# Kernel tuning notes

Measured on AMD Instinct MI355X. Metric: run time of the kernel, lower is better.

Reference implementation:

```python
import jax, jax.numpy as jnp
import numpy as np

MAX_PERIOD = 10000.0


def _rope(x, ts):
    # x: [B,H,T,D], ts: [B,T] integer positions (per-batch offset + arange(T))
    B, H, T, D = x.shape
    half = D // 2
    freqs = jnp.exp(jnp.arange(half, dtype=jnp.float32) * (-np.log(MAX_PERIOD) * 2.0 / D))
    ang = ts.astype(jnp.float32)[:, None, :, None] * freqs  # [B,1,T,half]
    cos, sin = jnp.cos(ang), jnp.sin(ang)
    xr = x.reshape(B, H, T, half, 2)  # interleaved (real, imag) pairs
    r, i = xr[..., 0], xr[..., 1]
    out = jnp.stack([r * cos - i * sin, r * sin + i * cos], axis=-1)
    return out.reshape(B, H, T, D)


def setup_inputs() -> dict:
    key = jax.random.key(0)
    ks = jax.random.split(key, 7)
    B, T, C = 8, 128, 1024
    H, D, CAP = 16, 64, 2048
    return {
        'x': jax.random.normal(ks[0], (B, T, C), dtype=jnp.float32),
        'w_in': jax.random.normal(ks[1], (3 * C, C), dtype=jnp.float32) * 0.02,
        'w_out': jax.random.normal(ks[2], (C, C), dtype=jnp.float32) * 0.02,
        'cache_k': jax.random.normal(ks[3], (B, H, CAP, D), dtype=jnp.float32),
        'cache_v': jax.random.normal(ks[4], (B, H, CAP, D), dtype=jnp.float32),
        'end_offset': jax.random.randint(ks[5], (B,), 0, CAP).astype(jnp.int64) if jax.config.jax_enable_x64 else jax.random.randint(ks[5], (B,), 0, CAP),
        'exec_mask': jnp.ones((B,), dtype=bool),
    }


def reference(x, w_in, w_out, cache_k, cache_v, end_offset, exec_mask):
    B, T, C = x.shape
    H, CAP = cache_k.shape[1], cache_k.shape[2]
    D = C // H
    context = CAP  # capacity == self.context

    # fused in-projection, split per rearrange 'b t (p h d) -> p b h t d', p=3
    qkv = (x @ w_in.T).reshape(B, T, 3, H, D).transpose(2, 0, 3, 1, 4)
    q, k, v = qkv[0], qkv[1], qkv[2]  # each [B,H,T,D]

    ts = end_offset[:, None] + jnp.arange(T)  # [B,T] absolute positions of new tokens
    q = _rope(q, ts)
    k = _rope(k, ts)

    # ring-buffer scatter (RingKVCache.complete)
    idx = ts % CAP  # [B,T]
    bI = jnp.arange(B)[:, None, None]
    hI = jnp.arange(H)[None, :, None]
    cache_k = cache_k.at[bI, hI, idx[:, None, :]].set(k)
    cache_v = cache_v.at[bI, hI, idx[:, None, :]].set(v)

    # absolute position of every cache slot, -1 for invalid slots
    cap_idx = jnp.arange(CAP)
    last = end_offset + T - 1  # [B]
    end_index = last % CAP
    delta = cap_idx[None, :] - end_index[:, None]  # [B,CAP]
    positions = jnp.where(delta <= 0, last[:, None] + delta, last[:, None] + delta - CAP)
    new_end = jnp.where(exec_mask, end_offset + T, end_offset)
    positions = jnp.where(cap_idx[None, :] >= new_end[:, None], -1, positions)

    # causal + context mask derived from positions
    d = ts[:, :, None] - positions[:, None, :]  # [B,T,CAP]
    mask = (positions[:, None, :] >= 0) & (d >= 0) & (d < context)

    scale = 1.0 / np.sqrt(D)
    scores = jnp.einsum('bhtd,bhsd->bhts', q, cache_k) * scale  # [B,H,T,CAP]
    scores = jnp.where(mask[:, None], scores, jnp.asarray(-1e9, scores.dtype))
    attn = jax.nn.softmax(scores, axis=-1)
    out = jnp.einsum('bhts,bhsd->bhtd', attn, cache_v)
    out = out.transpose(0, 2, 1, 3).reshape(B, T, C)  # 'b h t d -> b t (h d)'
    return out @ w_out.T
```

## Files before the change

kernel.cpp:

```cpp
#include <hip/hip_runtime.h>
#include <math.h>

#define BB 8
#define TT 128
#define CC 1024
#define HH 16
#define DD 64
#define CAP 2048
#define NSPLIT 4

typedef __attribute__((ext_vector_type(8))) short short8;
typedef __attribute__((ext_vector_type(4))) short short4v;
typedef __attribute__((ext_vector_type(4))) float float4v;
typedef _Float16 half8 __attribute__((ext_vector_type(8)));
typedef _Float16 half4v __attribute__((ext_vector_type(4)));

__device__ __forceinline__ short f2bf(float x) {
    union { float f; unsigned u; } un; un.f = x;
    unsigned r = (un.u + 0x7FFF + ((un.u >> 16) & 1)) >> 16;
    return (short)r;
}
__device__ __forceinline__ unsigned cvt_pk_bf16(float a, float b) {
    unsigned r;
    asm("v_cvt_pk_bf16_f32 %0, %1, %2" : "=v"(r) : "v"(a), "v"(b));
    return r;
}

__global__ __launch_bounds__(256) void split_all(const float* __restrict__ x,
                                                 const float* __restrict__ w_in,
                                                 const float* __restrict__ w_out,
                                                 _Float16* __restrict__ xhi,
                                                 _Float16* __restrict__ xlo,
                                                 _Float16* __restrict__ wh,
                                                 _Float16* __restrict__ woh) {
    size_t i = ((size_t)blockIdx.x * 256 + threadIdx.x) * 4;
    if (i < (size_t)1048576) {
        float4 f = *(const float4*)(x + i);
        half4v h, l;
        h.x = (_Float16)f.x; l.x = (_Float16)(f.x - (float)h.x);
        h.y = (_Float16)f.y; l.y = (_Float16)(f.y - (float)h.y);
        h.z = (_Float16)f.z; l.z = (_Float16)(f.z - (float)h.z);
        h.w = (_Float16)f.w; l.w = (_Float16)(f.w - (float)h.w);
        *(half4v*)(xhi + i) = h;
        *(half4v*)(xlo + i) = l;
    } else if (i < (size_t)4194304) {
        size_t off = i - 1048576;
        float4 f = *(const float4*)(w_in + off);
        half4v h;
        h.x = (_Float16)f.x; h.y = (_Float16)f.y; h.z = (_Float16)f.z; h.w = (_Float16)f.w;
        *(half4v*)(wh + off) = h;
    } else {
        size_t off = i - 4194304;
        float4 f = *(const float4*)(w_out + off);
        half4v h;
        h.x = (_Float16)f.x; h.y = (_Float16)f.y; h.z = (_Float16)f.z; h.w = (_Float16)f.w;
        *(half4v*)(woh + off) = h;
    }
}

template <int ROWS>
__device__ __forceinline__ void stage_glds(const unsigned short* __restrict__ src,
                                           unsigned short* lds, int K, int wv, int lane) {
#pragma unroll
    for (int c = wv; c < ROWS / 16; c += 4) {
        int row = c * 16 + (lane >> 2);
        int g = lane & 3;
        const unsigned short* ga = src + (size_t)row * K + g * 8;
        unsigned short* la = lds + c * 512 + lane * 8;
        __builtin_amdgcn_global_load_lds((__attribute__((address_space(1))) const unsigned short*)ga,
                                         (__attribute__((address_space(3))) unsigned short*)la,
                                         16, 0, 0);
    }
}

template <int MT, int NT>
__global__ __launch_bounds__(256) void gemm_f16x2(const _Float16* __restrict__ Ahi,
                                                  const _Float16* __restrict__ Alo,
                                                  const _Float16* __restrict__ Bh,
                                                  float* __restrict__ C, int M, int N, int K) {
    constexpr int BM = 2 * MT * 16, BN = 2 * NT * 16;
    __shared__ __align__(16) _Float16 As_h[BM * 32];
    __shared__ __align__(16) _Float16 As_l[BM * 32];
    __shared__ __align__(16) _Float16 Bs[BN * 32];

    int tid = threadIdx.x;
    int lane = tid & 63, wv = tid >> 6;
    int wr = wv >> 1, wc = wv & 1;
    int quad = lane >> 4, lq = lane & 15;
    int m0 = blockIdx.y * BM, n0 = blockIdx.x * BN;

    float4v acc[MT][NT];
#pragma unroll
    for (int mt = 0; mt < MT; ++mt)
#pragma unroll
        for (int nt = 0; nt < NT; ++nt) acc[mt][nt] = (float4v){0.f, 0.f, 0.f, 0.f};

    const unsigned short* a_h = (const unsigned short*)(Ahi + (size_t)m0 * K);
    const unsigned short* a_l = (const unsigned short*)(Alo + (size_t)m0 * K);
    const unsigned short* b_h = (const unsigned short*)(Bh + (size_t)n0 * K);

    for (int k0 = 0; k0 < K; k0 += 32) {
        __syncthreads();
        stage_glds<BM>(a_h + k0, (unsigned short*)As_h, K, wv, lane);
        stage_glds<BM>(a_l + k0, (unsigned short*)As_l, K, wv, lane);
        stage_glds<BN>(b_h + k0, (unsigned short*)Bs, K, wv, lane);
        __syncthreads();

        half8 ah[MT], al[MT];
#pragma unroll
        for (int mt = 0; mt < MT; ++mt) {
            int row = wr * MT * 16 + mt * 16 + lq;
            ah[mt] = *(const half8*)&As_h[row * 32 + quad * 8];
            al[mt] = *(const half8*)&As_l[row * 32 + quad * 8];
        }
#pragma unroll
        for (int nt = 0; nt < NT; ++nt) {
            int row = wc * NT * 16 + nt * 16 + lq;
            half8 bh = *(const half8*)&Bs[row * 32 + quad * 8];
#pragma unroll
            for (int mt = 0; mt < MT; ++mt) {
                float4v c = acc[mt][nt];
                c = __builtin_amdgcn_mfma_f32_16x16x32_f16(ah[mt], bh, c, 0, 0, 0);
                c = __builtin_amdgcn_mfma_f32_16x16x32_f16(al[mt], bh, c, 0, 0, 0);
                acc[mt][nt] = c;
            }
        }
    }

#pragma unroll
    for (int mt = 0; mt < MT; ++mt)
#pragma unroll
        for (int nt = 0; nt < NT; ++nt) {
            int n = n0 + wc * NT * 16 + nt * 16 + lq;
#pragma unroll
            for (int r = 0; r < 4; ++r) {
                int m = m0 + wr * MT * 16 + mt * 16 + quad * 4 + r;
                C[(size_t)m * N + n] = acc[mt][nt][r];
            }
        }
}

__global__ __launch_bounds__(256) void rope_scatter(const float* __restrict__ qkv,
                                                    unsigned short* __restrict__ q_bf,
                                                    float* __restrict__ cache_k,
                                                    float* __restrict__ cache_v,
                                                    const int* __restrict__ end_offset) {
    int gid = blockIdx.x * 256 + threadIdx.x;
    int j = gid & 31;
    int h = (gid >> 5) & 15;
    int t = (gid >> 9) & 127;
    int b = gid >> 16;

    int ts = end_offset[b] + t;
    int slot = ts & (CAP - 1);

    float freq = expf(-0.28782313662425574f * (float)j);
    float ang = (float)ts * freq;
    float s, c;
    sincosf(ang, &s, &c);

    const float* base = qkv + (size_t)(b * TT + t) * (3 * CC);
    int col = h * DD + 2 * j;
    float2 qv = *(const float2*)&base[col];
    float2 kv = *(const float2*)&base[CC + col];
    float2 vv = *(const float2*)&base[2 * CC + col];

    float qr = qv.x * c - qv.y * s;
    float qi = qv.x * s + qv.y * c;
    float kr = kv.x * c - kv.y * s;
    float ki = kv.x * s + kv.y * c;

    size_t qo = ((size_t)(b * HH + h) * TT + t) * DD + 2 * j;
    ushort2 qp;
    qp.x = (unsigned short)f2bf(qr * 0.125f);
    qp.y = (unsigned short)f2bf(qi * 0.125f);
    *(ushort2*)&q_bf[qo] = qp;
    size_t ko = ((size_t)(b * HH + h) * CAP + slot) * DD + 2 * j;
    *(float2*)&cache_k[ko] = make_float2(kr, ki);
    *(float2*)&cache_v[ko] = vv;
}

__global__ __launch_bounds__(256) void attn_mfma(const unsigned short* __restrict__ qb,
                                                 const float* __restrict__ ck,
                                                 const float* __restrict__ cv,
                                                 const int* __restrict__ endo,
                                                 const unsigned char* __restrict__ emb,
                                                 const int* __restrict__ emi,
                                                 float* __restrict__ pacc012,
                                                 float* __restrict__ pacc3,
                                                 float* __restrict__ pml) {
    __shared__ __align__(16) short k_s[64 * 72];
    __shared__ __align__(16) short v_t[64 * 64];
    __shared__ __align__(16) short p_s[4][16 * 72];

    int tid = threadIdx.x;
    int lane = tid & 63, wv = tid >> 6;
    int quad = lane >> 4, lq = lane & 15;
    int f = blockIdx.x + 128 * (blockIdx.y + 2 * blockIdx.z);
    int sid = f & 3;
    int qc2 = (f >> 2) & 1;
    int hb = f >> 3;
    int h = hb & 15, b = hb >> 4;
    int qrow = qc2 * 64 + wv * 16 + lq;

    int end0 = endo[b];
    int em = (emb[b] != 0) || (emi[b] != 0);
    int last = end0 + TT - 1;
    int end_index = last & (CAP - 1);
    int new_end = em ? (end0 + TT) : end0;
    int se = new_end < CAP ? new_end : CAP;
    int ntiles = (se + 63) >> 6;

    int tq = end0 + qrow;
    int tq0 = end0 + qc2 * 64 + wv * 16;
    int len_bad = last - tq0;
    int a_bad = (tq0 + 1) & (CAP - 1);

    const unsigned short* qrp = qb + ((size_t)(b * HH + h) * TT + qrow) * DD;
    short8 aq0 = *(const short8*)(qrp + quad * 8);
    short8 aq1 = *(const short8*)(qrp + 32 + quad * 8);

    const float* kg = ck + (size_t)(b * HH + h) * CAP * DD;
    const float* vg = cv + (size_t)(b * HH + h) * CAP * DD;

    int k_row = tid >> 4, k_f4 = tid & 15;
    float4 kreg[4];
    float vreg[2][8];

    float m = 0.f, l = 0.f;
    float4v acc[4];
#pragma unroll
    for (int mt = 0; mt < 4; ++mt) acc[mt] = (float4v){0.f, 0.f, 0.f, 0.f};

    if (sid < ntiles) {
        int sb = sid * 64;
#pragma unroll
        for (int i = 0; i < 4; ++i)
            kreg[i] = *(const float4*)&kg[(size_t)(sb + k_row + 16 * i) * DD + k_f4 * 4];
#pragma unroll
        for (int gi = 0; gi < 2; ++gi) {
            int g = wv + gi * 4;
#pragma unroll
            for (int i = 0; i < 8; ++i)
                vreg[gi][i] = vg[(size_t)(sb + g * 8 + i) * DD + lane];
        }
    }

    for (int t = sid; t < ntiles; t += NSPLIT) {
        int s0 = t * 64;
        __syncthreads();
#pragma unroll
        for (int i = 0; i < 4; ++i) {
            float4 fv = kreg[i];
            uint2 u;
            u.x = cvt_pk_bf16(fv.x, fv.y);
            u.y = cvt_pk_bf16(fv.z, fv.w);
            *(uint2*)&k_s[(k_row + 16 * i) * 72 + k_f4 * 4] = u;
        }
#pragma unroll
        for (int gi = 0; gi < 2; ++gi) {
            int g = wv + gi * 4;
            uint4 u;
            u.x = cvt_pk_bf16(vreg[gi][0], vreg[gi][1]);
            u.y = cvt_pk_bf16(vreg[gi][2], vreg[gi][3]);
            u.z = cvt_pk_bf16(vreg[gi][4], vreg[gi][5]);
            u.w = cvt_pk_bf16(vreg[gi][6], vreg[gi][7]);
            *(uint4*)&v_t[lane * 64 + (g ^ (lane & 7)) * 8] = u;
        }
        __syncthreads();
        int tn = t + NSPLIT;
        if (tn < ntiles) {
            int sn = tn * 64;
#pragma unroll
            for (int i = 0; i < 4; ++i)
                kreg[i] = *(const float4*)&kg[(size_t)(sn + k_row + 16 * i) * DD + k_f4 * 4];
#pragma unroll
            for (int gi = 0; gi < 2; ++gi) {
                int g = wv + gi * 4;
#pragma unroll
                for (int i = 0; i < 8; ++i)
                    vreg[gi][i] = vg[(size_t)(sn + g * 8 + i) * DD + lane];
            }
        }

        float4v sc[4];
#pragma unroll
        for (int nt = 0; nt < 4; ++nt) {
            const short* kr = &k_s[(nt * 16 + lq) * 72 + quad * 8];
            short8 bk0 = *(const short8*)kr;
            short8 bk1 = *(const short8*)(kr + 32);
            float4v c = (float4v){0.f, 0.f, 0.f, 0.f};
            c = __builtin_amdgcn_mfma_f32_16x16x32_bf16(bk0, aq0, c, 0, 0, 0);
            c = __builtin_amdgcn_mfma_f32_16x16x32_bf16(bk1, aq1, c, 0, 0, 0);
            sc[nt] = c;
        }

        int off = (s0 - a_bad) & (CAP - 1);
        bool fast = (off >= len_bad) && (off <= CAP - 64) && (s0 + 63 < se);
        float x[4][4];
        if (fast) {
#pragma unroll
            for (int nt = 0; nt < 4; ++nt)
#pragma unroll
                for (int r = 0; r < 4; ++r) x[nt][r] = sc[nt][r];
        } else {
#pragma unroll
            for (int nt = 0; nt < 4; ++nt)
#pragma unroll
                for (int r = 0; r < 4; ++r) {
                    int s = s0 + nt * 16 + quad * 4 + r;
                    int delta = s - end_index;
                    int pos = (delta <= 0) ? (last + delta) : (last + delta - CAP);
                    bool valid = (s < se) && (pos <= tq);
                    x[nt][r] = valid ? sc[nt][r] : -1.0e30f;
                }
        }

        float v01 = fmaxf(fmaxf(x[0][0], x[0][1]), fmaxf(x[0][2], x[0][3]));
        float v23 = fmaxf(fmaxf(x[1][0], x[1][1]), fmaxf(x[1][2], x[1][3]));
        float v45 = fmaxf(fmaxf(x[2][0], x[2][1]), fmaxf(x[2][2], x[2][3]));
        float v67 = fmaxf(fmaxf(x[3][0], x[3][1]), fmaxf(x[3][2], x[3][3]));
        float vm = fmaxf(fmaxf(v01, v23), fmaxf(v45, v67));
        vm = fmaxf(vm, __shfl_xor(vm, 16, 64));
        vm = fmaxf(vm, __shfl_xor(vm, 32, 64));
        float mn = fmaxf(m, vm);
        float al = __expf(m - mn);
        float ps = 0.f;
#pragma unroll
        for (int nt = 0; nt < 4; ++nt)
#pragma unroll
            for (int r = 0; r < 4; ++r) {
                float p = __expf(x[nt][r] - mn);
                x[nt][r] = p;
                ps += p;
            }
        ps += __shfl_xor(ps, 16, 64);
        ps += __shfl_xor(ps, 32, 64);
        l = l * al + ps;
        m = mn;

#pragma unroll
        for (int nt = 0; nt < 4; ++nt) {
            uint2 u;
            u.x = cvt_pk_bf16(x[nt][0], x[nt][1]);
            u.y = cvt_pk_bf16(x[nt][2], x[nt][3]);
            *(uint2*)&p_s[wv][lq * 72 + nt * 16 + quad * 4] = u;
        }

        short8 bp0 = *(const short8*)&p_s[wv][lq * 72 + quad * 8];
        short8 bp1 = *(const short8*)&p_s[wv][lq * 72 + 32 + quad * 8];
#pragma unroll
        for (int mt = 0; mt < 4; ++mt) {
            int d = mt * 16 + lq;
            const short* vr = &v_t[d * 64];
            short8 av0 = *(const short8*)(vr + ((quad ^ (d & 7)) * 8));
            short8 av1 = *(const short8*)(vr + (((4 + quad) ^ (d & 7)) * 8));
            float4v a = acc[mt];
            a.x *= al; a.y *= al; a.z *= al; a.w *= al;
            a = __builtin_amdgcn_mfma_f32_16x16x32_bf16(av0, bp0, a, 0, 0, 0);
            a = __builtin_amdgcn_mfma_f32_16x16x32_bf16(av1, bp1, a, 0, 0, 0);
            acc[mt] = a;
        }
    }

    int base_row = (b * HH + h) * TT + qc2 * 64;
    float* pa = (sid < 3) ? (pacc012 + (size_t)sid * (16384 * 64)) : pacc3;
    int row_g = base_row + wv * 16 + lq;
#pragma unroll
    for (int mt = 0; mt < 4; ++mt)
        *(float4v*)&pa[(size_t)row_g * 64 + mt * 16 + quad * 4] = acc[mt];
    if (quad == 0) {
        size_t ix = ((size_t)sid * 16384 + row_g) * 2;
        pml[ix] = m;
        pml[ix + 1] = l;
    }
}

__global__ __launch_bounds__(256) void attn_combine(const float* __restrict__ pacc012,
                                                    const float* __restrict__ pacc3,
                                                    const float* __restrict__ pml,
                                                    _Float16* __restrict__ ahi,
                                                    _Float16* __restrict__ alo) {
    int gid = blockIdx.x * 256 + threadIdx.x;
    int row = gid >> 6, d = gid & 63;

    float mv[NSPLIT], lv[NSPLIT];
#pragma unroll
    for (int s = 0; s < NSPLIT; ++s) {
        size_t ix = ((size_t)s * 16384 + row) * 2;
        mv[s] = pml[ix];
        lv[s] = pml[ix + 1];
    }
    float M = fmaxf(fmaxf(mv[0], mv[1]), fmaxf(mv[2], mv[3]));
    float O = 0.f, L = 0.f;
#pragma unroll
    for (int s = 0; s < NSPLIT; ++s) {
        const float* pa = (s < 3) ? (pacc012 + (size_t)s * (16384 * 64)) : pacc3;
        float w = __expf(mv[s] - M);
        L += w * lv[s];
        O += w * pa[(size_t)row * 64 + d];
    }
    float o = (L > 0.f) ? (O / L) : 0.f;

    int b = row >> 11, h = (row >> 7) & 15, q = row & 127;
    size_t ob = ((size_t)(b * TT + q)) * CC + h * DD + d;
    _Float16 hi = (_Float16)o;
    ahi[ob] = hi;
    alo[ob] = (_Float16)(o - (float)hi);
}

extern "C" void kernel_launch(void* const* d_in, const int* in_sizes, int n_in,
                              void* d_out, int out_size, void* d_ws, size_t ws_size,
                              hipStream_t stream) {
    const float* x = (const float*)d_in[0];
    const float* w_in = (const float*)d_in[1];
    const float* w_out = (const float*)d_in[2];
    float* cache_k = (float*)d_in[3];
    float* cache_v = (float*)d_in[4];
    const int* end_offset = (const int*)d_in[5];
    const unsigned char* exec_mask_b = (const unsigned char*)d_in[6];
    const int* exec_mask_i = (const int*)d_in[6];
    float* out = (float*)d_out;

    float* qkv = (float*)d_ws;
    unsigned short* q_bf = (unsigned short*)(qkv + (size_t)1024 * 3072);
    _Float16* xhi = (_Float16*)(q_bf + (size_t)1024 * 1024);
    _Float16* xlo = xhi + (size_t)1024 * 1024;
    _Float16* wh = xlo + (size_t)1024 * 1024;
    _Float16* woh = wh + (size_t)3072 * 1024;
    _Float16* ahi = woh + (size_t)1024 * 1024;
    _Float16* alo = ahi + (size_t)1024 * 1024;

    float* pacc012 = qkv;
    float* pacc3 = (float*)xhi;
    float* pml = (float*)wh;

    split_all<<<5120, 256, 0, stream>>>(x, w_in, w_out, xhi, xlo, wh, woh);
    gemm_f16x2<2, 2><<<dim3(3072 / 64, 1024 / 64), 256, 0, stream>>>(
        xhi, xlo, wh, qkv, BB * TT, 3 * CC, CC);
    rope_scatter<<<(BB * TT * HH * 32) / 256, 256, 0, stream>>>(qkv, q_bf, cache_k, cache_v, end_offset);
    attn_mfma<<<dim3(HH * BB, 2, NSPLIT), 256, 0, stream>>>(q_bf, cache_k, cache_v, end_offset,
                                                            exec_mask_b, exec_mask_i,
                                                            pacc012, pacc3, pml);
    attn_combine<<<(16384 * 64) / 256, 256, 0, stream>>>(pacc012, pacc3, pml, ahi, alo);
    gemm_f16x2<1, 2><<<dim3(1024 / 64, 1024 / 32), 256, 0, stream>>>(
        ahi, alo, woh, out, BB * TT, CC, CC);
}
```

Before: 223.7 us.

## Split attention KV range eight ways and read new K/V from a side buffer

When the workspace is large enough, rotated K and V for the new tokens go to a compact side buffer instead of being scattered into the input caches. The attention kernel then redirects ring slots holding new tokens to that buffer. The KV loop is split eight ways instead of four, giving more blocks to fill the GPU, and the combine step skips empty splits. The QKV and output GEMM tile shapes are also retuned. The costs are extra address arithmetic per loaded row, larger partial-result buffers, and a fallback path that depends on workspace size.

```diff
diff --git a/kernel.cpp b/kernel.cpp
--- a/kernel.cpp
+++ b/kernel.cpp
@@ -7,7 +7,6 @@
 #define HH 16
 #define DD 64
 #define CAP 2048
-#define NSPLIT 4
 
 typedef __attribute__((ext_vector_type(8))) short short8;
 typedef __attribute__((ext_vector_type(4))) short short4v;
@@ -142,9 +141,10 @@
 
 __global__ __launch_bounds__(256) void rope_scatter(const float* __restrict__ qkv,
                                                     unsigned short* __restrict__ q_bf,
-                                                    float* __restrict__ cache_k,
-                                                    float* __restrict__ cache_v,
-                                                    const int* __restrict__ end_offset) {
+                                                    float* __restrict__ dk,
+                                                    float* __restrict__ dv,
+                                                    const int* __restrict__ end_offset,
+                                                    int ring) {
     int gid = blockIdx.x * 256 + threadIdx.x;
     int j = gid & 31;
     int h = (gid >> 5) & 15;
@@ -175,31 +175,36 @@
     qp.x = (unsigned short)f2bf(qr * 0.125f);
     qp.y = (unsigned short)f2bf(qi * 0.125f);
     *(ushort2*)&q_bf[qo] = qp;
-    size_t ko = ((size_t)(b * HH + h) * CAP + slot) * DD + 2 * j;
-    *(float2*)&cache_k[ko] = make_float2(kr, ki);
-    *(float2*)&cache_v[ko] = vv;
-}
-
+    size_t ko = ring ? (((size_t)(b * HH + h) * CAP + slot) * DD + 2 * j)
+                     : (((size_t)(b * HH + h) * TT + t) * DD + 2 * j);
+    *(float2*)&dk[ko] = make_float2(kr, ki);
+    *(float2*)&dv[ko] = vv;
+}
+
+template <int NS, bool NOMUT>
 __global__ __launch_bounds__(256) void attn_mfma(const unsigned short* __restrict__ qb,
                                                  const float* __restrict__ ck,
                                                  const float* __restrict__ cv,
+                                                 const float* __restrict__ knew,
+                                                 const float* __restrict__ vnew,
                                                  const int* __restrict__ endo,
                                                  const unsigned char* __restrict__ emb,
                                                  const int* __restrict__ emi,
-                                                 float* __restrict__ pacc012,
-                                                 float* __restrict__ pacc3,
+                                                 float* __restrict__ pacc_a,
+                                                 float* __restrict__ pacc_b,
                                                  float* __restrict__ pml) {
     __shared__ __align__(16) short k_s[64 * 72];
     __shared__ __align__(16) short v_t[64 * 64];
     __shared__ __align__(16) short p_s[4][16 * 72];
 
+    constexpr int LS = (NS == 8) ? 3 : 2;
     int tid = threadIdx.x;
     int lane = tid & 63, wv = tid >> 6;
     int quad = lane >> 4, lq = lane & 15;
     int f = blockIdx.x + 128 * (blockIdx.y + 2 * blockIdx.z);
-    int sid = f & 3;
-    int qc2 = (f >> 2) & 1;
-    int hb = f >> 3;
+    int sid = f & (NS - 1);
+    int qc2 = (f >> LS) & 1;
+    int hb = f >> (LS + 1);
     int h = hb & 15, b = hb >> 4;
     int qrow = qc2 * 64 + wv * 16 + lq;
 
@@ -215,6 +220,7 @@
     int tq0 = end0 + qc2 * 64 + wv * 16;
     int len_bad = last - tq0;
     int a_bad = (tq0 + 1) & (CAP - 1);
+    int a_new = end0 & (CAP - 1);
 
     const unsigned short* qrp = qb + ((size_t)(b * HH + h) * TT + qrow) * DD;
     short8 aq0 = *(const short8*)(qrp + quad * 8);
@@ -222,31 +228,57 @@
 
     const float* kg = ck + (size_t)(b * HH + h) * CAP * DD;
     const float* vg = cv + (size_t)(b * HH + h) * CAP * DD;
+    const float* kn = NOMUT ? (knew + (size_t)(b * HH + h) * TT * DD) : nullptr;
+    const float* vn = NOMUT ? (vnew + (size_t)(b * HH + h) * TT * DD) : nullptr;
 
     int k_row = tid >> 4, k_f4 = tid & 15;
     float4 kreg[4];
     float vreg[2][8];
 
+    auto ldK = [&](int sb) {
+#pragma unroll
+        for (int i = 0; i < 4; ++i) {
+            int s = sb + k_row + 16 * i;
+            const float* src;
+            if constexpr (NOMUT) {
+                int on = (s - a_new) & (CAP - 1);
+                src = (on < TT) ? (kn + (size_t)on * DD) : (kg + (size_t)s * DD);
+            } else {
+                src = kg + (size_t)s * DD;
+            }
+            kreg[i] = *(const float4*)&src[k_f4 * 4];
+        }
+    };
+    auto ldV = [&](int sb) {
+#pragma unroll
+        for (int gi = 0; gi < 2; ++gi) {
+            int g = wv + gi * 4;
+#pragma unroll
+            for (int i = 0; i < 8; ++i) {
+                int s = sb + g * 8 + i;
+                const float* src;
+                if constexpr (NOMUT) {
+                    int on = (s - a_new) & (CAP - 1);
+                    src = (on < TT) ? (vn + (size_t)on * DD) : (vg + (size_t)s * DD);
+                } else {
+                    src = vg + (size_t)s * DD;
+                }
+                vreg[gi][i] = src[lane];
+            }
+        }
+    };
+
     float m = 0.f, l = 0.f;
     float4v acc[4];
 #pragma unroll
     for (int mt = 0; mt < 4; ++mt) acc[mt] = (float4v){0.f, 0.f, 0.f, 0.f};
 
     if (sid < ntiles) {
-        int sb = sid * 64;
-#pragma unroll
-        for (int i = 0; i < 4; ++i)
-            kreg[i] = *(const float4*)&kg[(size_t)(sb + k_row + 16 * i) * DD + k_f4 * 4];
-#pragma unroll
-        for (int gi = 0; gi < 2; ++gi) {
-            int g = wv + gi * 4;
-#pragma unroll
-            for (int i = 0; i < 8; ++i)
-                vreg[gi][i] = vg[(size_t)(sb + g * 8 + i) * DD + lane];
-        }
-    }
-
-    for (int t = sid; t < ntiles; t += NSPLIT) {
+        ldK(sid * 64);
+        ldV(sid * 64);
+    }
+
+    for (int t = sid; t < ntiles; t += NS) {
         int s0 = t * 64;
         __syncthreads();
 #pragma unroll
@@ -268,19 +300,9 @@
             *(uint4*)&v_t[lane * 64 + (g ^ (lane & 7)) * 8] = u;
         }
         __syncthreads();
-        int tn = t + NSPLIT;
-        if (tn < ntiles) {
-            int sn = tn * 64;
-#pragma unroll
-            for (int i = 0; i < 4; ++i)
-                kreg[i] = *(const float4*)&kg[(size_t)(sn + k_row + 16 * i) * DD + k_f4 * 4];
-#pragma unroll
-            for (int gi = 0; gi < 2; ++gi) {
-                int g = wv + gi * 4;
-#pragma unroll
-                for (int i = 0; i < 8; ++i)
-                    vreg[gi][i] = vg[(size_t)(sn + g * 8 + i) * DD + lane];
-            }
+        if (t + NS < ntiles) {
+            ldK((t + NS) * 64);
+            ldV((t + NS) * 64);
         }
 
         float4v sc[4];
@@ -364,11 +386,17 @@
     }
 
     int base_row = (b * HH + h) * TT + qc2 * 64;
-    float* pa = (sid < 3) ? (pacc012 + (size_t)sid * (16384 * 64)) : pacc3;
+    float* pa;
+    if constexpr (NS == 4)
+        pa = (sid < 3) ? (pacc_a + (size_t)sid * (16384 * 64)) : pacc_b;
+    else
+        pa = pacc_a + (size_t)sid * (16384 * 64);
     int row_g = base_row + wv * 16 + lq;
-#pragma unroll
-    for (int mt = 0; mt < 4; ++mt)
-        *(float4v*)&pa[(size_t)row_g * 64 + mt * 16 + quad * 4] = acc[mt];
+    if (sid < ntiles) {
+#pragma unroll
+        for (int mt = 0; mt < 4; ++mt)
+            *(float4v*)&pa[(size_t)row_g * 64 + mt * 16 + quad * 4] = acc[mt];
+    }
     if (quad == 0) {
         size_t ix = ((size_t)sid * 16384 + row_g) * 2;
         pml[ix] = m;
@@ -376,29 +404,38 @@
     }
 }
 
-__global__ __launch_bounds__(256) void attn_combine(const float* __restrict__ pacc012,
-                                                    const float* __restrict__ pacc3,
+template <int NS>
+__global__ __launch_bounds__(256) void attn_combine(const float* __restrict__ pacc_a,
+                                                    const float* __restrict__ pacc_b,
                                                     const float* __restrict__ pml,
                                                     _Float16* __restrict__ ahi,
                                                     _Float16* __restrict__ alo) {
     int gid = blockIdx.x * 256 + threadIdx.x;
     int row = gid >> 6, d = gid & 63;
 
-    float mv[NSPLIT], lv[NSPLIT];
-#pragma unroll
-    for (int s = 0; s < NSPLIT; ++s) {
+    float mv[NS], lv[NS];
+#pragma unroll
+    for (int s = 0; s < NS; ++s) {
         size_t ix = ((size_t)s * 16384 + row) * 2;
         mv[s] = pml[ix];
         lv[s] = pml[ix + 1];
     }
-    float M = fmaxf(fmaxf(mv[0], mv[1]), fmaxf(mv[2], mv[3]));
+    float M = mv[0];
+#pragma unroll
+    for (int s = 1; s < NS; ++s) M = fmaxf(M, mv[s]);
     float O = 0.f, L = 0.f;
 #pragma unroll
-    for (int s = 0; s < NSPLIT; ++s) {
-        const float* pa = (s < 3) ? (pacc012 + (size_t)s * (16384 * 64)) : pacc3;
-        float w = __expf(mv[s] - M);
-        L += w * lv[s];
-        O += w * pa[(size_t)row * 64 + d];
+    for (int s = 0; s < NS; ++s) {
+        if (lv[s] > 0.f) {
+            const float* pa;
+            if constexpr (NS == 4)
+                pa = (s < 3) ? (pacc_a + (size_t)s * (16384 * 64)) : pacc_b;
+            else
+                pa = pacc_a + (size_t)s * (16384 * 64);
+            float w = __expf(mv[s] - M);
+            L += w * lv[s];
+            O += w * pa[(size_t)row * 64 + d];
+        }
     }
     float o = (L > 0.f) ? (O / L) : 0.f;
 
@@ -422,27 +459,46 @@
     const int* exec_mask_i = (const int*)d_in[6];
     float* out = (float*)d_out;
 
-    float* qkv = (float*)d_ws;
-    unsigned short* q_bf = (unsigned short*)(qkv + (size_t)1024 * 3072);
-    _Float16* xhi = (_Float16*)(q_bf + (size_t)1024 * 1024);
-    _Float16* xlo = xhi + (size_t)1024 * 1024;
-    _Float16* wh = xlo + (size_t)1024 * 1024;
-    _Float16* woh = wh + (size_t)3072 * 1024;
-    _Float16* ahi = woh + (size_t)1024 * 1024;
-    _Float16* alo = ahi + (size_t)1024 * 1024;
-
-    float* pacc012 = qkv;
-    float* pacc3 = (float*)xhi;
-    float* pml = (float*)wh;
+    const size_t MB = 1024 * 1024;
+    char* w = (char*)d_ws;
+    float* qkv = (float*)w;
+    unsigned short* q_bf = (unsigned short*)(w + 12 * MB);
+    _Float16* xhi = (_Float16*)(w + 14 * MB);
+    _Float16* xlo = (_Float16*)(w + 16 * MB);
+    _Float16* wh  = (_Float16*)(w + 18 * MB);
+    _Float16* woh = (_Float16*)(w + 24 * MB);
+    _Float16* ahi = (_Float16*)(w + 26 * MB);
+    _Float16* alo = (_Float16*)(w + 28 * MB);
+
+    bool big = ws_size >= 72 * MB;
 
     split_all<<<5120, 256, 0, stream>>>(x, w_in, w_out, xhi, xlo, wh, woh);
-    gemm_f16x2<2, 2><<<dim3(3072 / 64, 1024 / 64), 256, 0, stream>>>(
+    gemm_f16x2<2, 4><<<dim3(3072 / 128, 1024 / 64), 256, 0, stream>>>(
         xhi, xlo, wh, qkv, BB * TT, 3 * CC, CC);
-    rope_scatter<<<(BB * TT * HH * 32) / 256, 256, 0, stream>>>(qkv, q_bf, cache_k, cache_v, end_offset);
-    attn_mfma<<<dim3(HH * BB, 2, NSPLIT), 256, 0, stream>>>(q_bf, cache_k, cache_v, end_offset,
-                                                            exec_mask_b, exec_mask_i,
-                                                            pacc012, pacc3, pml);
-    attn_combine<<<(16384 * 64) / 256, 256, 0, stream>>>(pacc012, pacc3, pml, ahi, alo);
-    gemm_f16x2<1, 2><<<dim3(1024 / 64, 1024 / 32), 256, 0, stream>>>(
+
+    if (big) {
+        float* knew = (float*)(w + 30 * MB);
+        float* vnew = (float*)(w + 34 * MB);
+        float* pacc = (float*)(w + 38 * MB);
+        float* pml  = (float*)(w + 70 * MB);
+        rope_scatter<<<(BB * TT * HH * 32) / 256, 256, 0, stream>>>(
+            qkv, q_bf, knew, vnew, end_offset, 0);
+        attn_mfma<8, true><<<dim3(HH * BB, 2, 8), 256, 0, stream>>>(
+            q_bf, cache_k, cache_v, knew, vnew, end_offset,
+            exec_mask_b, exec_mask_i, pacc, nullptr, pml);
+        attn_combine<8><<<(16384 * 64) / 256, 256, 0, stream>>>(pacc, nullptr, pml, ahi, alo);
+    } else {
+        float* pacc012 = qkv;
+        float* pacc3 = (float*)xhi;
+        float* pml = (float*)wh;
+        rope_scatter<<<(BB * TT * HH * 32) / 256, 256, 0, stream>>>(
+            qkv, q_bf, cache_k, cache_v, end_offset, 1);
+        attn_mfma<4, false><<<dim3(HH * BB, 2, 4), 256, 0, stream>>>(
+            q_bf, cache_k, cache_v, nullptr, nullptr, end_offset,
+            exec_mask_b, exec_mask_i, pacc012, pacc3, pml);
+        attn_combine<4><<<(16384 * 64) / 256, 256, 0, stream>>>(pacc012, pacc3, pml, ahi, alo);
+    }
+
+    gemm_f16x2<2, 2><<<dim3(1024 / 64, 1024 / 64), 256, 0, stream>>>(
         ahi, alo, woh, out, BB * TT, CC, CC);
 }
```

After: 233.6 us. 4.4% more time.

## Load-balance split-K attention by per-batch valid tile count; retile GEMMs

Applied to the files above, without the earlier changes.

The attention kernel no longer uses a fixed 4-way interleaved split. It now assigns contiguous chunks of TPB key tiles per block, with the grid mapped from each batch's valid cache length, so blocks for short batches are not launched. When the workspace is large enough it uses 4-tile chunks and a dedicated partial buffer holding up to 8 splits; the combine kernel reads only the splits that exist. The QKV and output GEMM tile shapes are also changed. This is meant to cut wasted blocks and improve balance, at the cost of a per-block scan over the batches and more partial-buffer traffic.

```diff
diff --git a/kernel.cpp b/kernel.cpp
--- a/kernel.cpp
+++ b/kernel.cpp
@@ -7,7 +7,6 @@
 #define HH 16
 #define DD 64
 #define CAP 2048
-#define NSPLIT 4
 
 typedef __attribute__((ext_vector_type(8))) short short8;
 typedef __attribute__((ext_vector_type(4))) short short4v;
@@ -180,14 +179,15 @@
     *(float2*)&cache_v[ko] = vv;
 }
 
+template <int TPB, bool FBK>
 __global__ __launch_bounds__(256) void attn_mfma(const unsigned short* __restrict__ qb,
                                                  const float* __restrict__ ck,
                                                  const float* __restrict__ cv,
                                                  const int* __restrict__ endo,
                                                  const unsigned char* __restrict__ emb,
                                                  const int* __restrict__ emi,
-                                                 float* __restrict__ pacc012,
-                                                 float* __restrict__ pacc3,
+                                                 float* __restrict__ pacc_a,
+                                                 float* __restrict__ pacc_b,
                                                  float* __restrict__ pml) {
     __shared__ __align__(16) short k_s[64 * 72];
     __shared__ __align__(16) short v_t[64 * 64];
@@ -196,20 +196,36 @@
     int tid = threadIdx.x;
     int lane = tid & 63, wv = tid >> 6;
     int quad = lane >> 4, lq = lane & 15;
-    int f = blockIdx.x + 128 * (blockIdx.y + 2 * blockIdx.z);
-    int sid = f & 3;
-    int qc2 = (f >> 2) & 1;
-    int hb = f >> 3;
-    int h = hb & 15, b = hb >> 4;
+
+    int f = blockIdx.x;
+    int b = -1, rem = 0, ntiles = 0;
+    int cum = 0;
+#pragma unroll
+    for (int bb = 0; bb < 8; ++bb) {
+        int e0 = endo[bb];
+        int emx = (emb[bb] != 0) || (emi[bb] != 0);
+        int ne = emx ? (e0 + TT) : e0;
+        int seb = ne < CAP ? ne : CAP;
+        int ntb = (seb + 63) >> 6;
+        int nsb = (ntb + TPB - 1) / TPB;
+        int wbl = 32 * nsb;
+        if (b < 0 && f < cum + wbl) { b = bb; rem = f - cum; ntiles = ntb; }
+        cum += wbl;
+    }
+    if (b < 0) return;
+    int sid = rem >> 5;
+    int hq = rem & 31;
+    int h = hq & 15, qc2 = hq >> 4;
+    int tstart = sid * TPB;
+    int tend = tstart + TPB < ntiles ? tstart + TPB : ntiles;
+
     int qrow = qc2 * 64 + wv * 16 + lq;
-
     int end0 = endo[b];
     int em = (emb[b] != 0) || (emi[b] != 0);
     int last = end0 + TT - 1;
     int end_index = last & (CAP - 1);
     int new_end = em ? (end0 + TT) : end0;
     int se = new_end < CAP ? new_end : CAP;
-    int ntiles = (se + 63) >> 6;
 
     int tq = end0 + qrow;
     int tq0 = end0 + qc2 * 64 + wv * 16;
@@ -227,26 +243,30 @@
     float4 kreg[4];
     float vreg[2][8];
 
+    auto ldK = [&](int sb) {
+#pragma unroll
+        for (int i = 0; i < 4; ++i)
+            kreg[i] = *(const float4*)&kg[(size_t)(sb + k_row + 16 * i) * DD + k_f4 * 4];
+    };
+    auto ldV = [&](int sb) {
+#pragma unroll
+        for (int gi = 0; gi < 2; ++gi) {
+            int g = wv + gi * 4;
+#pragma unroll
+            for (int i = 0; i < 8; ++i)
+                vreg[gi][i] = vg[(size_t)(sb + g * 8 + i) * DD + lane];
+        }
+    };
+
     float m = 0.f, l = 0.f;
     float4v acc[4];
 #pragma unroll
     for (int mt = 0; mt < 4; ++mt) acc[mt] = (float4v){0.f, 0.f, 0.f, 0.f};
 
-    if (sid < ntiles) {
-        int sb = sid * 64;
-#pragma unroll
-        for (int i = 0; i < 4; ++i)
-            kreg[i] = *(const float4*)&kg[(size_t)(sb + k_row + 16 * i) * DD + k_f4 * 4];
-#pragma unroll
-        for (int gi = 0; gi < 2; ++gi) {
-            int g = wv + gi * 4;
-#pragma unroll
-            for (int i = 0; i < 8; ++i)
-                vreg[gi][i] = vg[(size_t)(sb + g * 8 + i) * DD + lane];
-        }
-    }
-
-    for (int t = sid; t < ntiles; t += NSPLIT) {
+    ldK(tstart * 64);
+    ldV(tstart * 64);
+
+    for (int t = tstart; t < tend; ++t) {
         int s0 = t * 64;
         __syncthreads();
 #pragma unroll
@@ -268,19 +288,9 @@
             *(uint4*)&v_t[lane * 64 + (g ^ (lane & 7)) * 8] = u;
         }
         __syncthreads();
-        int tn = t + NSPLIT;
-        if (tn < ntiles) {
-            int sn = tn * 64;
-#pragma unroll
-            for (int i = 0; i < 4; ++i)
-                kreg[i] = *(const float4*)&kg[(size_t)(sn + k_row + 16 * i) * DD + k_f4 * 4];
-#pragma unroll
-            for (int gi = 0; gi < 2; ++gi) {
-                int g = wv + gi * 4;
-#pragma unroll
-                for (int i = 0; i < 8; ++i)
-                    vreg[gi][i] = vg[(size_t)(sn + g * 8 + i) * DD + lane];
-            }
+        if (t + 1 < tend) {
+            ldK((t + 1) * 64);
+            ldV((t + 1) * 64);
         }
 
         float4v sc[4];
@@ -364,7 +374,11 @@
     }
 
     int base_row = (b * HH + h) * TT + qc2 * 64;
-    float* pa = (sid < 3) ? (pacc012 + (size_t)sid * (16384 * 64)) : pacc3;
+    float* pa;
+    if constexpr (FBK)
+        pa = (sid < 3) ? (pacc_a + (size_t)sid * (16384 * 64)) : pacc_b;
+    else
+        pa = pacc_a + (size_t)sid * (16384 * 64);
     int row_g = base_row + wv * 16 + lq;
 #pragma unroll
     for (int mt = 0; mt < 4; ++mt)
@@ -376,34 +390,58 @@
     }
 }
 
-__global__ __launch_bounds__(256) void attn_combine(const float* __restrict__ pacc012,
-                                                    const float* __restrict__ pacc3,
+template <int TPB, bool FBK>
+__global__ __launch_bounds__(256) void attn_combine(const float* __restrict__ pacc_a,
+                                                    const float* __restrict__ pacc_b,
                                                     const float* __restrict__ pml,
+                                                    const int* __restrict__ endo,
+                                                    const unsigned char* __restrict__ emb,
+                                                    const int* __restrict__ emi,
                                                     _Float16* __restrict__ ahi,
                                                     _Float16* __restrict__ alo) {
+    constexpr int MAXS = FBK ? 4 : 8;
     int gid = blockIdx.x * 256 + threadIdx.x;
     int row = gid >> 6, d = gid & 63;
-
-    float mv[NSPLIT], lv[NSPLIT];
-#pragma unroll
-    for (int s = 0; s < NSPLIT; ++s) {
-        size_t ix = ((size_t)s * 16384 + row) * 2;
-        mv[s] = pml[ix];
-        lv[s] = pml[ix + 1];
-    }
-    float M = fmaxf(fmaxf(mv[0], mv[1]), fmaxf(mv[2], mv[3]));
+    int b = row >> 11;
+
+    int e0 = endo[b];
+    int emx = (emb[b] != 0) || (emi[b] != 0);
+    int ne = emx ? (e0 + TT) : e0;
+    int seb = ne < CAP ? ne : CAP;
+    int ntb = (seb + 63) >> 6;
+    int ns = (ntb + TPB - 1) / TPB;
+
+    float mv[MAXS], lv[MAXS];
+#pragma unroll
+    for (int s = 0; s < MAXS; ++s) {
+        mv[s] = 0.f; lv[s] = 0.f;
+        if (s < ns) {
+            size_t ix = ((size_t)s * 16384 + row) * 2;
+            mv[s] = pml[ix];
+            lv[s] = pml[ix + 1];
+        }
+    }
+    float M = 0.f;
+#pragma unroll
+    for (int s = 0; s < MAXS; ++s) M = fmaxf(M, mv[s]);
     float O = 0.f, L = 0.f;
 #pragma unroll
-    for (int s = 0; s < NSPLIT; ++s) {
-        const float* pa = (s < 3) ? (pacc012 + (size_t)s * (16384 * 64)) : pacc3;
-        float w = __expf(mv[s] - M);
-        L += w * lv[s];
-        O += w * pa[(size_t)row * 64 + d];
+    for (int s = 0; s < MAXS; ++s) {
+        if (s < ns && lv[s] > 0.f) {
+            const float* pa;
+            if constexpr (FBK)
+                pa = (s < 3) ? (pacc_a + (size_t)s * (16384 * 64)) : pacc_b;
+            else
+                pa = pacc_a + (size_t)s * (16384 * 64);
+            float w = __expf(mv[s] - M);
+            L += w * lv[s];
+            O += w * pa[(size_t)row * 64 + d];
+        }
     }
     float o = (L > 0.f) ? (O / L) : 0.f;
 
-    int b = row >> 11, h = (row >> 7) & 15, q = row & 127;
-    size_t ob = ((size_t)(b * TT + q)) * CC + h * DD + d;
+    int bq = row >> 11, h = (row >> 7) & 15, q = row & 127;
+    size_t ob = ((size_t)(bq * TT + q)) * CC + h * DD + d;
     _Float16 hi = (_Float16)o;
     ahi[ob] = hi;
     alo[ob] = (_Float16)(o - (float)hi);
@@ -422,27 +460,44 @@
     const int* exec_mask_i = (const int*)d_in[6];
     float* out = (float*)d_out;
 
-    float* qkv = (float*)d_ws;
-    unsigned short* q_bf = (unsigned short*)(qkv + (size_t)1024 * 3072);
-    _Float16* xhi = (_Float16*)(q_bf + (size_t)1024 * 1024);
-    _Float16* xlo = xhi + (size_t)1024 * 1024;
-    _Float16* wh = xlo + (size_t)1024 * 1024;
-    _Float16* woh = wh + (size_t)3072 * 1024;
-    _Float16* ahi = woh + (size_t)1024 * 1024;
-    _Float16* alo = ahi + (size_t)1024 * 1024;
-
-    float* pacc012 = qkv;
-    float* pacc3 = (float*)xhi;
-    float* pml = (float*)wh;
+    const size_t MB = 1024 * 1024;
+    char* w = (char*)d_ws;
+    float* qkv = (float*)w;
+    unsigned short* q_bf = (unsigned short*)(w + 12 * MB);
+    _Float16* xhi = (_Float16*)(w + 14 * MB);
+    _Float16* xlo = (_Float16*)(w + 16 * MB);
+    _Float16* wh  = (_Float16*)(w + 18 * MB);
+    _Float16* woh = (_Float16*)(w + 24 * MB);
+    _Float16* ahi = (_Float16*)(w + 26 * MB);
+    _Float16* alo = (_Float16*)(w + 28 * MB);
+
+    bool big = ws_size >= 72 * MB;
 
     split_all<<<5120, 256, 0, stream>>>(x, w_in, w_out, xhi, xlo, wh, woh);
-    gemm_f16x2<2, 2><<<dim3(3072 / 64, 1024 / 64), 256, 0, stream>>>(
+    gemm_f16x2<2, 4><<<dim3(3072 / 128, 1024 / 64), 256, 0, stream>>>(
         xhi, xlo, wh, qkv, BB * TT, 3 * CC, CC);
-    rope_scatter<<<(BB * TT * HH * 32) / 256, 256, 0, stream>>>(qkv, q_bf, cache_k, cache_v, end_offset);
-    attn_mfma<<<dim3(HH * BB, 2, NSPLIT), 256, 0, stream>>>(q_bf, cache_k, cache_v, end_offset,
-                                                            exec_mask_b, exec_mask_i,
-                                                            pacc012, pacc3, pml);
-    attn_combine<<<(16384 * 64) / 256, 256, 0, stream>>>(pacc012, pacc3, pml, ahi, alo);
-    gemm_f16x2<1, 2><<<dim3(1024 / 64, 1024 / 32), 256, 0, stream>>>(
+    rope_scatter<<<(BB * TT * HH * 32) / 256, 256, 0, stream>>>(
+        qkv, q_bf, cache_k, cache_v, end_offset);
+
+    if (big) {
+        float* pacc = (float*)(w + 38 * MB);
+        float* pml  = (float*)(w + 70 * MB);
+        attn_mfma<4, false><<<2048, 256, 0, stream>>>(
+            q_bf, cache_k, cache_v, end_offset, exec_mask_b, exec_mask_i,
+            pacc, nullptr, pml);
+        attn_combine<4, false><<<(16384 * 64) / 256, 256, 0, stream>>>(
+            pacc, nullptr, pml, end_offset, exec_mask_b, exec_mask_i, ahi, alo);
+    } else {
+        float* pacc012 = qkv;
+        float* pacc3 = (float*)xhi;
+        float* pml = (float*)wh;
+        attn_mfma<8, true><<<1024, 256, 0, stream>>>(
+            q_bf, cache_k, cache_v, end_offset, exec_mask_b, exec_mask_i,
+            pacc012, pacc3, pml);
+        attn_combine<8, true><<<(16384 * 64) / 256, 256, 0, stream>>>(
+            pacc012, pacc3, pml, end_offset, exec_mask_b, exec_mask_i, ahi, alo);
+    }
+
+    gemm_f16x2<2, 2><<<dim3(1024 / 64, 1024 / 64), 256, 0, stream>>>(
         ahi, alo, woh, out, BB * TT, CC, CC);
 }
```

Measured after the change: 232.8 us. +4.1%, slower.
